# Performance work log

Hardware: AMD Instinct MI355X
Metric: run time of the kernel (lower is better)

The kernel has to match this reference:

```python
import jax, jax.numpy as jnp
import numpy as np

C = 512
H_HEADS = 8
CTX_D = 768
GEO_D = 512
FFN_D = 4 * C
EPS = 1e-5


def _layernorm(x, g, b):
    mu = jnp.mean(x, axis=-1, keepdims=True)
    var = jnp.mean((x - mu) ** 2, axis=-1, keepdims=True)
    return (x - mu) * jax.lax.rsqrt(var + EPS) * g + b


def _cross_attn(x, ctx, Wq, Wk, Wv, Wo, bo, h):
    # x: (B, N, C), ctx: (B, S, Dctx)
    b, n, _ = x.shape
    s = ctx.shape[1]
    inner = Wq.shape[1]
    d = inner // h
    q = (x @ Wq).reshape(b, n, h, d)
    k = (ctx @ Wk).reshape(b, s, h, d)
    v = (ctx @ Wv).reshape(b, s, h, d)
    sim = jnp.einsum('bihd,bjhd->bhij', q, k) * (d ** -0.5)
    attn = jax.nn.softmax(sim, axis=-1)
    out = jnp.einsum('bhij,bjhd->bihd', attn, v).reshape(b, n, inner)
    return out @ Wo + bo


def setup_inputs() -> dict:
    key = jax.random.key(0)
    ks = jax.random.split(key, 24)
    std = lambda fan_in: 1.0 / np.sqrt(fan_in)
    inp = {
        'x': jax.random.normal(ks[0], (4, C, 64, 64), jnp.float32),
        'context': jax.random.normal(ks[1], (4, 77, CTX_D), jnp.float32),
        'geometry_tokens': jax.random.normal(ks[2], (4, 256, GEO_D), jnp.float32),
        # layernorm params (norm1..norm4)
        'g1': jnp.ones((C,)), 'b1': jnp.zeros((C,)),
        'g2': jnp.ones((C,)), 'b2': jnp.zeros((C,)),
        'g3': jnp.ones((C,)), 'b3': jnp.zeros((C,)),
        'g4': jnp.ones((C,)), 'b4': jnp.zeros((C,)),
        # cross-attention (context) weights
        'cWq': jax.random.normal(ks[3], (C, C)) * std(C),
        'cWk': jax.random.normal(ks[4], (CTX_D, C)) * std(CTX_D),
        'cWv': jax.random.normal(ks[5], (CTX_D, C)) * std(CTX_D),
        'cWo': jax.random.normal(ks[6], (C, C)) * std(C),
        'cbo': jnp.zeros((C,)),
        # geometry-attention weights
        'gWq': jax.random.normal(ks[7], (C, C)) * std(C),
        'gWk': jax.random.normal(ks[8], (GEO_D, C)) * std(GEO_D),
        'gWv': jax.random.normal(ks[9], (GEO_D, C)) * std(GEO_D),
        'gWo': jax.random.normal(ks[10], (C, C)) * std(C),
        'gbo': jnp.zeros((C,)),
        # FFN weights
        'W1': jax.random.normal(ks[11], (C, FFN_D)) * std(C),
        'bf1': jnp.zeros((FFN_D,)),
        'W2': jax.random.normal(ks[12], (FFN_D, C)) * std(FFN_D),
        'bf2': jnp.zeros((C,)),
    }
    return inp


def reference(x, context, geometry_tokens,
              g1, b1, g2, b2, g3, b3, g4, b4,
              cWq, cWk, cWv, cWo, cbo,
              gWq, gWk, gWv, gWo, gbo,
              W1, bf1, W2, bf2):
    b, c, h, w = x.shape
    t = x.reshape(b, c, h * w).transpose(0, 2, 1)  # (B, N, C)
    # self_attn is called with context=None -> identity, so this is t + norm1(t)
    t = t + _layernorm(t, g1, b1)
    t = t + _cross_attn(_layernorm(t, g2, b2), context, cWq, cWk, cWv, cWo, cbo, H_HEADS)
    t = t + _cross_attn(_layernorm(t, g3, b3), geometry_tokens, gWq, gWk, gWv, gWo, gbo, H_HEADS)
    hdn = jax.nn.gelu(_layernorm(t, g4, b4) @ W1 + bf1, approximate=False)
    t = t + hdn @ W2 + bf2
    return t.transpose(0, 2, 1).reshape(b, c, h, w)
```

## Files before the change

kernel.cpp:

```cpp
#include <hip/hip_runtime.h>
#include <hip/hip_bf16.h>

using bf16 = __hip_bfloat16;
typedef __attribute__((ext_vector_type(8))) short short8;
typedef __attribute__((ext_vector_type(4))) short short4v;
typedef __attribute__((ext_vector_type(4))) float floatx4;

#define DEVFN __device__ __forceinline__

DEVFN float bf2f(bf16 v) { return __bfloat162float(v); }
DEVFN bf16 f2bf(float v) { return __float2bfloat16(v); }
DEVFN float us2f(unsigned short u) {
    union { unsigned int i; float f; } c; c.i = ((unsigned int)u) << 16; return c.f;
}
DEVFN unsigned short f2bfbits(float v) {
    union { bf16 h; unsigned short u; } c; c.h = f2bf(v); return c.u;
}
DEVFN float loadF(const void* p, size_t i, int isf) {
    return isf ? ((const float*)p)[i] : us2f(((const unsigned short*)p)[i]);
}
DEVFN void gl_lds16(const bf16* g, short* l) {
    __builtin_amdgcn_global_load_lds(
        (const __attribute__((address_space(1))) unsigned int*)g,
        (__attribute__((address_space(3))) unsigned int*)l, 16, 0, 0);
}
DEVFN float fast_gelu(float v) {
    float u = v * (0.7978845608028654f + 0.0356774081f * v * v);
    float e = __expf(2.f * u);
    float th = 1.f - 2.f / (e + 1.f);
    return 0.5f * v * (1.f + th);
}

__global__ __launch_bounds__(256) void detect_kernel(const void* x, int* flag)
{
    __shared__ int any;
    if (threadIdx.x == 0) any = 0;
    __syncthreads();
    const unsigned short* p = (const unsigned short*)x;
    int hit = 0;
    for (int i = threadIdx.x; i < 8192; i += 256) {
        if ((p[i] & 0x7F80u) == 0x7F80u) hit = 1;
    }
    if (hit) any = 1;
    __syncthreads();
    if (threadIdx.x == 0) flag[0] = any;
}

struct CVTab {
    const void* src[14];
    bf16* dst[14];
    int cnt[14];
    int bstart[14];
};
__global__ __launch_bounds__(256) void convert_batch_kernel(
    CVTab tab, const int* __restrict__ flag)
{
    int isf = *flag;
    int b = blockIdx.x;
    int s = 0;
#pragma unroll
    for (int i = 1; i < 14; i++) if (b >= tab.bstart[i]) s = i;
    const void* src = tab.src[s];
    bf16* dst = tab.dst[s];
    int cnt = tab.cnt[s];
    int base = (b - tab.bstart[s]) * 2048;
    int lim = min(base + 2048, cnt);
    for (int i = base + (int)threadIdx.x; i < lim; i += 256)
        dst[i] = f2bf(loadF(src, i, isf));
}

__global__ __launch_bounds__(256) void ln_in_kernel(
    const void* __restrict__ x, float* __restrict__ t,
    const bf16* __restrict__ g, const bf16* __restrict__ bta,
    const int* __restrict__ flag, int NN)
{
    __shared__ float tile[16][516];
    int isf = *flag;
    int b = blockIdx.y;
    int n0 = blockIdx.x * 16;
    int tid = threadIdx.x;
    int nx = tid & 15, cy = tid >> 4;
#pragma unroll
    for (int p = 0; p < 32; p++) {
        int c = p * 16 + cy;
        tile[nx][c] = loadF(x, ((size_t)b * 512 + c) * NN + n0 + nx, isf);
    }
    __syncthreads();
    int w = tid >> 6, lane = tid & 63;
    for (int rr = 0; rr < 4; rr++) {
        int r = w * 4 + rr;
        float4 v0 = *(const float4*)&tile[r][lane * 8];
        float4 v1 = *(const float4*)&tile[r][lane * 8 + 4];
        float vals[8] = {v0.x, v0.y, v0.z, v0.w, v1.x, v1.y, v1.z, v1.w};
        float s = 0.f;
#pragma unroll
        for (int i = 0; i < 8; i++) s += vals[i];
#pragma unroll
        for (int off = 32; off; off >>= 1) s += __shfl_xor(s, off, 64);
        float mu = s * (1.f / 512.f);
        float sq = 0.f;
#pragma unroll
        for (int i = 0; i < 8; i++) { float d = vals[i] - mu; sq += d * d; }
#pragma unroll
        for (int off = 32; off; off >>= 1) sq += __shfl_xor(sq, off, 64);
        float rs = rsqrtf(sq * (1.f / 512.f) + 1e-5f);
        float out[8];
#pragma unroll
        for (int i = 0; i < 8; i++) {
            int c = lane * 8 + i;
            out[i] = vals[i] + (vals[i] - mu) * rs * bf2f(g[c]) + bf2f(bta[c]);
        }
        float* tp = t + ((size_t)b * NN + n0 + r) * 512 + lane * 8;
        *(float4*)tp = make_float4(out[0], out[1], out[2], out[3]);
        *(float4*)(tp + 4) = make_float4(out[4], out[5], out[6], out[7]);
    }
}

__global__ __launch_bounds__(256) void transpose_out_kernel(
    const float* __restrict__ t, void* __restrict__ o, const int* __restrict__ flag,
    int C, int NN)
{
    __shared__ float tile[32][33];
    int isf = *flag;
    int b = blockIdx.z;
    int n0 = blockIdx.x * 32, c0 = blockIdx.y * 32;
    int tx = threadIdx.x, ty = threadIdx.y;
#pragma unroll
    for (int i = 0; i < 4; i++)
        tile[ty + i * 8][tx] = __builtin_nontemporal_load(
            &t[((size_t)b * NN + n0 + ty + i * 8) * C + c0 + tx]);
    __syncthreads();
#pragma unroll
    for (int i = 0; i < 4; i++) {
        size_t oi = ((size_t)b * C + c0 + ty + i * 8) * NN + n0 + tx;
        float val = tile[tx][ty + i * 8];
        if (isf) ((float*)o)[oi] = val;
        else ((bf16*)o)[oi] = f2bf(val);
    }
}

struct TWTab {
    const void* src[10];
    bf16* dst[10];
    int K[10];
    int Nc[10];
    int tstart[10];
};
__global__ __launch_bounds__(256) void transpose_w_batch(
    TWTab tab, const int* __restrict__ flag)
{
    __shared__ float tile[32][33];
    int isf = *flag;
    int b = blockIdx.x;
    int s = 0;
#pragma unroll
    for (int i = 1; i < 10; i++) if (b >= tab.tstart[i]) s = i;
    const void* Wm = tab.src[s];
    bf16* WT = tab.dst[s];
    int K = tab.K[s], Nc = tab.Nc[s];
    int lt = b - tab.tstart[s];
    int ntx = Nc >> 5;
    int n0 = (lt % ntx) * 32, k0 = (lt / ntx) * 32;
    int tx = threadIdx.x, ty = threadIdx.y;
#pragma unroll
    for (int i = 0; i < 4; i++)
        tile[ty + i * 8][tx] = loadF(Wm, (size_t)(k0 + ty + i * 8) * Nc + n0 + tx, isf);
    __syncthreads();
#pragma unroll
    for (int i = 0; i < 4; i++)
        WT[(size_t)(n0 + ty + i * 8) * K + k0 + tx] = f2bf(tile[tx][ty + i * 8]);
}

__global__ __launch_bounds__(256) void ln_kernel(
    const float* __restrict__ t, const bf16* __restrict__ g, const bf16* __restrict__ bta,
    bf16* __restrict__ outp, int Mrows)
{
    int w = threadIdx.x >> 6, lane = threadIdx.x & 63;
    int row = blockIdx.x * 4 + w;
    if (row >= Mrows) return;
    const float* xr = t + (size_t)row * 512;
    floatx4 v0 = __builtin_nontemporal_load((const floatx4*)(xr + lane * 8));
    floatx4 v1 = __builtin_nontemporal_load((const floatx4*)(xr + lane * 8 + 4));
    float vals[8] = {v0[0], v0[1], v0[2], v0[3], v1[0], v1[1], v1[2], v1[3]};
    float s = 0.f;
#pragma unroll
    for (int i = 0; i < 8; i++) s += vals[i];
#pragma unroll
    for (int off = 32; off; off >>= 1) s += __shfl_xor(s, off, 64);
    float mu = s * (1.f / 512.f);
    float sq = 0.f;
#pragma unroll
    for (int i = 0; i < 8; i++) { float d = vals[i] - mu; sq += d * d; }
#pragma unroll
    for (int off = 32; off; off >>= 1) sq += __shfl_xor(sq, off, 64);
    float rs = rsqrtf(sq * (1.f / 512.f) + 1e-5f);
#pragma unroll
    for (int i = 0; i < 8; i++) {
        int c = lane * 8 + i;
        float y = (vals[i] - mu) * rs * bf2f(g[c]) + bf2f(bta[c]);
        outp[(size_t)row * 512 + c] = f2bf(y);
    }
}

template <int MODE>
__global__ __launch_bounds__(256) void gemm64x2(
    const bf16* __restrict__ A,
    const bf16* __restrict__ WT0, const bf16* __restrict__ WT1,
    bf16* __restrict__ o0, bf16* __restrict__ o1,
    int M, int K, int Nc)
{
    const bf16* WT = blockIdx.z ? WT1 : WT0;
    bf16* outp = blockIdx.z ? o1 : o0;
    __shared__ short As[64 * 32];
    __shared__ short Bs[64 * 32];
    const int tid = threadIdx.x;
    const int m0 = blockIdx.y * 64;
    const int n0 = blockIdx.x * 64;
    const int w = tid >> 6;
    const int lane = tid & 63;
    const int lm = lane & 15;
    const int lq = lane >> 4;

    floatx4 acc[4];
#pragma unroll
    for (int nb = 0; nb < 4; nb++) acc[nb] = (floatx4){0.f, 0.f, 0.f, 0.f};

    const int srow = tid >> 2;
    const int scol = (tid & 3) << 3;
    const int agrow = m0 + srow;
    const bool aok = agrow < M;
    const bf16* Aptr = A + (size_t)agrow * K + scol;
    const bf16* Bptr = WT + (size_t)(n0 + srow) * K + scol;

    for (int k0 = 0; k0 < K; k0 += 32) {
        __syncthreads();
        int4 av = make_int4(0, 0, 0, 0);
        if (aok) av = *(const int4*)(Aptr + k0);
        *(int4*)(&As[srow * 32 + scol]) = av;
        *(int4*)(&Bs[srow * 32 + scol]) = *(const int4*)(Bptr + k0);
        __syncthreads();
        short8 a = *(const short8*)(&As[(w * 16 + lm) * 32 + lq * 8]);
#pragma unroll
        for (int nb = 0; nb < 4; nb++) {
            short8 b = *(const short8*)(&Bs[(nb * 16 + lm) * 32 + lq * 8]);
            acc[nb] = __builtin_amdgcn_mfma_f32_16x16x32_bf16(a, b, acc[nb], 0, 0, 0);
        }
    }

#pragma unroll
    for (int nb = 0; nb < 4; nb++) {
        int col = n0 + nb * 16 + lm;
#pragma unroll
        for (int r = 0; r < 4; r++) {
            int row = m0 + w * 16 + lq * 4 + r;
            if (row < M) {
                float v = acc[nb][r];
                if (MODE == 1) v = fast_gelu(v);
                outp[(size_t)row * Nc + col] = f2bf(v);
            }
        }
    }
}

#define MFMA_PAIR(RB, A00, A01, A10, A11)                                              \
    _Pragma("unroll")                                                                   \
    for (int cb = 0; cb < CB; cb++) {                                                   \
        acc[cb][RB]     = __builtin_amdgcn_mfma_f32_16x16x32_bf16(bf0[cb], A00, acc[cb][RB], 0, 0, 0);     \
        acc[cb][RB]     = __builtin_amdgcn_mfma_f32_16x16x32_bf16(bf1[cb], A01, acc[cb][RB], 0, 0, 0);     \
        acc[cb][RB + 1] = __builtin_amdgcn_mfma_f32_16x16x32_bf16(bf0[cb], A10, acc[cb][RB + 1], 0, 0, 0); \
        acc[cb][RB + 1] = __builtin_amdgcn_mfma_f32_16x16x32_bf16(bf1[cb], A11, acc[cb][RB + 1], 0, 0, 0); \
    }

template <int MODE, int CB>
__global__ __launch_bounds__(512, 2) void gemm8p(
    const bf16* __restrict__ A, const bf16* __restrict__ WT,
    const bf16* __restrict__ bias, void* __restrict__ outp,
    int K, int Nc)
{
    constexpr int BN = CB * 64;
    constexpr int ABUF = 256 * 64;
    constexpr int BBUF = BN * 64;
    __shared__ short As[2 * ABUF];
    __shared__ short Bs[2 * BBUF];

    const int tid = threadIdx.x;
    const int gx = gridDim.x;
    int g = blockIdx.y * gx + blockIdx.x;
    const int cpx = (gx * gridDim.y) >> 3;
    g = (g & 7) * cpx + (g >> 3);
    const int m0 = (g / gx) * 256;
    const int n0 = (g % gx) * BN;

    const int w = tid >> 6, lane = tid & 63;
    const int lm = lane & 15, lq = lane >> 4;
    const int wm = w >> 2, wn = w & 3;

    floatx4 acc[CB][8];
#pragma unroll
    for (int cb = 0; cb < CB; cb++)
#pragma unroll
        for (int rb = 0; rb < 8; rb++) acc[cb][rb] = (floatx4){0.f, 0.f, 0.f, 0.f};

    const int rbaseA = (tid >> 3) + ((tid >= 256) ? 96 : 0);
    const int chk = (((tid & 7) ^ ((tid >> 3) & 7)) << 3);
    const bf16* pA = A + (size_t)(m0 + rbaseA) * K + chk;
    const int rbaseB = ((tid >> 7) << (CB == 4 ? 6 : 5)) + ((tid >> 3) & 15);
    const bf16* pB = WT + (size_t)(n0 + rbaseB) * K + chk;
    const int wbA = w * 512 + ((w >= 4) ? 6144 : 0);
    const int wbB = (CB == 4) ? ((w >> 1) * 4096 + (w & 1) * 512)
                              : ((w >> 1) * 2048 + (w & 1) * 512);
    const size_t K32 = (size_t)K * 32;
    const size_t K16 = (size_t)K * 16;

    const int arow = (wm * 128 + lm) * 64;
    const int brow = (wn * CB * 16 + lm) * 64;
    const int sl0 = ((lq ^ (lm & 7)) << 3);
    const int sl1 = (((4 + lq) ^ (lm & 7)) << 3);

    const int nt = K >> 6;

#pragma unroll
    for (int q = 0; q < 4; q++) gl_lds16(pA + (size_t)q * K32, As + q * 2048 + wbA);
    if constexpr (CB == 4) {
        gl_lds16(pB,           Bs + wbB);
        gl_lds16(pB + K16,     Bs + 1024 + wbB);
        gl_lds16(pB + 2 * K16, Bs + 2048 + wbB);
        gl_lds16(pB + 3 * K16, Bs + 3072 + wbB);
    } else {
        gl_lds16(pB,       Bs + wbB);
        gl_lds16(pB + K16, Bs + 1024 + wbB);
    }
    {
        const bf16* qA = pA + 64;
        const bf16* qB = pB + 64;
        if constexpr (CB == 4) {
            gl_lds16(qB,           Bs + BBUF + wbB);
            gl_lds16(qB + K16,     Bs + BBUF + 1024 + wbB);
            gl_lds16(qB + 2 * K16, Bs + BBUF + 2048 + wbB);
            gl_lds16(qB + 3 * K16, Bs + BBUF + 3072 + wbB);
            gl_lds16(qA,           As + ABUF + wbA);
            gl_lds16(qA + K32,     As + ABUF + 2048 + wbA);
            asm volatile("s_waitcnt vmcnt(6)\n\ts_barrier" ::: "memory");
        } else {
            gl_lds16(qB,           Bs + BBUF + wbB);
            gl_lds16(qB + K16, Bs + BBUF + 1024 + wbB);
            gl_lds16(qA,           As + ABUF + wbA);
            gl_lds16(qA + K32,     As + ABUF + 2048 + wbA);
            gl_lds16(qA + 2 * K32, As + ABUF + 4096 + wbA);
            asm volatile("s_waitcnt vmcnt(5)\n\ts_barrier" ::: "memory");
        }
    }

    for (int s = 0; s < nt; ++s) {
        const int cu = s & 1;
        const short* cA = As + cu * ABUF;
        const short* cB = Bs + cu * BBUF;
        short* oA = As + (cu ^ 1) * ABUF;
        short* sA = As + cu * ABUF;
        short* sB = Bs + cu * BBUF;
        const bf16* pA1 = pA + (s + 1) * 64;
        const bf16* pA2 = pA + (s + 2) * 64;
        const bf16* pB2 = pB + (s + 2) * 64;
        short8 bf0[CB], bf1[CB], x0, x1, y0, y1;

#pragma unroll
        for (int cb = 0; cb < CB; cb++) {
            bf0[cb] = *(const short8*)&cB[brow + cb * 1024 + sl0];
            bf1[cb] = *(const short8*)&cB[brow + cb * 1024 + sl1];
        }
        x0 = *(const short8*)&cA[arow + sl0];
        x1 = *(const short8*)&cA[arow + sl1];
        y0 = *(const short8*)&cA[arow + 1024 + sl0];
        y1 = *(const short8*)&cA[arow + 1024 + sl1];
        if (s + 1 < nt) {
            if constexpr (CB == 4) {
                gl_lds16(pA1 + 2 * K32, oA + 2 * 2048 + wbA);
                gl_lds16(pA1 + 3 * K32, oA + 3 * 2048 + wbA);
            } else {
                gl_lds16(pA1 + 3 * K32, oA + 3 * 2048 + wbA);
            }
        }
        asm volatile("s_barrier" ::: "memory");
        __builtin_amdgcn_s_setprio(1);
        MFMA_PAIR(0, x0, x1, y0, y1)
        __builtin_amdgcn_s_setprio(0);
        asm volatile("s_waitcnt lgkmcnt(0)\n\ts_barrier" ::: "memory");

        x0 = *(const short8*)&cA[arow + 2 * 1024 + sl0];
        x1 = *(const short8*)&cA[arow + 2 * 1024 + sl1];
        y0 = *(const short8*)&cA[arow + 3 * 1024 + sl0];
        y1 = *(const short8*)&cA[arow + 3 * 1024 + sl1];
        if (s + 2 < nt) {
            gl_lds16(pB2,       sB + wbB);
            gl_lds16(pB2 + K16, sB + 1024 + wbB);
        }
        asm volatile("s_barrier" ::: "memory");
        __builtin_amdgcn_s_setprio(1);
        MFMA_PAIR(2, x0, x1, y0, y1)
        __builtin_amdgcn_s_setprio(0);
        asm volatile("s_waitcnt lgkmcnt(0)\n\ts_barrier" ::: "memory");

        x0 = *(const short8*)&cA[arow + 4 * 1024 + sl0];
        x1 = *(const short8*)&cA[arow + 4 * 1024 + sl1];
        y0 = *(const short8*)&cA[arow + 5 * 1024 + sl0];
        y1 = *(const short8*)&cA[arow + 5 * 1024 + sl1];
        if (s + 2 < nt) {
            if constexpr (CB == 4) {
                gl_lds16(pB2 + 2 * K16, sB + 2048 + wbB);
                gl_lds16(pB2 + 3 * K16, sB + 3072 + wbB);
            } else {
                gl_lds16(pA2, sA + wbA);
            }
        }
        asm volatile("s_barrier" ::: "memory");
        __builtin_amdgcn_s_setprio(1);
        MFMA_PAIR(4, x0, x1, y0, y1)
        __builtin_amdgcn_s_setprio(0);
        asm volatile("s_waitcnt lgkmcnt(0)\n\ts_barrier" ::: "memory");

        x0 = *(const short8*)&cA[arow + 6 * 1024 + sl0];
        x1 = *(const short8*)&cA[arow + 6 * 1024 + sl1];
        y0 = *(const short8*)&cA[arow + 7 * 1024 + sl0];
        y1 = *(const short8*)&cA[arow + 7 * 1024 + sl1];
        if (s + 2 < nt) {
            if constexpr (CB == 4) {
                gl_lds16(pA2,       sA + wbA);
                gl_lds16(pA2 + K32, sA + 2048 + wbA);
            } else {
                gl_lds16(pA2 + K32,     sA + 2048 + wbA);
                gl_lds16(pA2 + 2 * K32, sA + 4096 + wbA);
            }
        }
        asm volatile("s_barrier" ::: "memory");
        __builtin_amdgcn_s_setprio(1);
        MFMA_PAIR(6, x0, x1, y0, y1)
        __builtin_amdgcn_s_setprio(0);
        if (s <= nt - 3) {
            if constexpr (CB == 4)
                asm volatile("s_waitcnt vmcnt(6) lgkmcnt(0)\n\ts_barrier" ::: "memory");
            else
                asm volatile("s_waitcnt vmcnt(5) lgkmcnt(0)\n\ts_barrier" ::: "memory");
        } else if (s == nt - 2) {
            asm volatile("s_waitcnt vmcnt(0) lgkmcnt(0)\n\ts_barrier" ::: "memory");
        } else {
            asm volatile("s_waitcnt lgkmcnt(0)\n\ts_barrier" ::: "memory");
        }
    }
    __syncthreads();

    float4 bias4[CB];
#pragma unroll
    for (int cb = 0; cb < CB; cb++) {
        if (bias) {
            const bf16* bp = bias + n0 + wn * (CB * 16) + cb * 16 + lq * 4;
            bias4[cb] = make_float4(bf2f(bp[0]), bf2f(bp[1]), bf2f(bp[2]), bf2f(bp[3]));
        } else {
            bias4[cb] = make_float4(0.f, 0.f, 0.f, 0.f);
        }
    }

    if constexpr (MODE == 2) {
        float* po = (float*)outp;
#pragma unroll
        for (int rb = 0; rb < 8; rb++) {
            size_t m = m0 + wm * 128 + rb * 16 + lm;
#pragma unroll
            for (int cb = 0; cb < CB; cb++) {
                float* p = po + m * Nc + n0 + wn * (CB * 16) + cb * 16 + lq * 4;
                floatx4 f = __builtin_nontemporal_load((const floatx4*)p);
                f[0] += acc[cb][rb][0] + bias4[cb].x;
                f[1] += acc[cb][rb][1] + bias4[cb].y;
                f[2] += acc[cb][rb][2] + bias4[cb].z;
                f[3] += acc[cb][rb][3] + bias4[cb].w;
                __builtin_nontemporal_store(f, (floatx4*)p);
            }
        }
    } else if constexpr (CB == 2) {
        unsigned short* op = (unsigned short*)outp;
#pragma unroll
        for (int rb = 0; rb < 8; rb++) {
            size_t m = m0 + wm * 128 + rb * 16 + lm;
#pragma unroll
            for (int cb = 0; cb < 2; cb++) {
                short4v pk;
#pragma unroll
                for (int r = 0; r < 4; r++) {
                    float vv = acc[cb][rb][r] + ((const float*)&bias4[cb])[r];
                    if (MODE == 1) vv = fast_gelu(vv);
                    pk[r] = (short)f2bfbits(vv);
                }
                *(short4v*)(op + m * Nc + n0 + wn * 32 + cb * 16 + lq * 4) = pk;
            }
        }
    } else {
        unsigned short* stgb = (unsigned short*)&As[w * 1024];
        unsigned short* op = (unsigned short*)outp;
#pragma unroll
        for (int rb = 0; rb < 8; rb++) {
#pragma unroll
            for (int cb = 0; cb < 4; cb++) {
                short4v pk;
#pragma unroll
                for (int r = 0; r < 4; r++) {
                    float vv = acc[cb][rb][r] + ((const float*)&bias4[cb])[r];
                    if (MODE == 1) vv = fast_gelu(vv);
                    pk[r] = (short)f2bfbits(vv);
                }
                int chunk = (cb * 2 + (lq >> 1)) ^ (lm & 7);
                *(short4v*)(&stgb[lm * 64 + chunk * 8 + (lq & 1) * 4]) = pk;
            }
#pragma unroll
            for (int p = 0; p < 2; p++) {
                int row = p * 8 + (lane >> 3);
                int chunk = lane & 7;
                short8 ov = *(const short8*)(&stgb[row * 64 + ((chunk ^ (row & 7)) * 8)]);
                size_t m = m0 + wm * 128 + rb * 16 + row;
                short8* dst = (short8*)(op + m * Nc + n0 + wn * 64 + chunk * 8);
                if (MODE == 1) __builtin_nontemporal_store(ov, dst);
                else *dst = ov;
            }
        }
    }
}

template <int SPAD, int SVALID>
__global__ __launch_bounds__(256) void attn_mfma_kernel(
    const bf16* __restrict__ q, const bf16* __restrict__ k, const bf16* __restrict__ v,
    bf16* __restrict__ o, int N)
{
    constexpr int MB = SPAD / 16;
    constexpr int KS = SPAD / 32;
    __shared__ unsigned short lds[SPAD * 64 + 64 * SPAD];
    unsigned short* Ks = lds;
    unsigned short* Vt = lds + SPAD * 64;
    unsigned short* Pw = lds;

    const int tid = threadIdx.x;
    const int b = blockIdx.x >> 3;
    const int h = blockIdx.x & 7;
    const int n0 = blockIdx.y * 64;
    const int w = tid >> 6, lane = tid & 63;
    const int lm = lane & 15, lq = lane >> 4;

    const unsigned short* kp = (const unsigned short*)k;
    const unsigned short* vp = (const unsigned short*)v;
    for (int idx = tid * 8; idx < SPAD * 64; idx += 2048) {
        int s = idx >> 6, d0 = idx & 63;
        short8 kv = {0, 0, 0, 0, 0, 0, 0, 0};
        short8 vv = {0, 0, 0, 0, 0, 0, 0, 0};
        if (s < SVALID) {
            size_t gb = ((size_t)(b * SVALID + s)) * 512 + h * 64 + d0;
            kv = *(const short8*)(kp + gb);
            vv = *(const short8*)(vp + gb);
        }
        int kc = (d0 >> 3) ^ (s & 7);
        *(short8*)(&Ks[s * 64 + kc * 8]) = kv;
        const unsigned short* vvp = (const unsigned short*)&vv;
#pragma unroll
        for (int i = 0; i < 8; i++) {
            int d = d0 + i;
            int sc = (s >> 3) ^ (d & 7);
            Vt[d * SPAD + sc * 8 + (s & 7)] = vvp[i];
        }
    }

    const int q0 = n0 + w * 16;
    const unsigned short* qp = (const unsigned short*)q;
    size_t qbase = ((size_t)(b * N + q0 + lm)) * 512 + h * 64 + lq * 8;
    short8 qf0 = *(const short8*)(qp + qbase);
    short8 qf1 = *(const short8*)(qp + qbase + 32);
    __syncthreads();

    floatx4 sacc[MB];
#pragma unroll
    for (int mb = 0; mb < MB; mb++) sacc[mb] = (floatx4){0.f, 0.f, 0.f, 0.f};
#pragma unroll
    for (int mb = 0; mb < MB; mb++) {
        int srow = mb * 16 + lm;
        short8 a0 = *(const short8*)(&Ks[srow * 64 + ((lq ^ (lm & 7)) * 8)]);
        short8 a1 = *(const short8*)(&Ks[srow * 64 + (((4 + lq) ^ (lm & 7)) * 8)]);
        sacc[mb] = __builtin_amdgcn_mfma_f32_16x16x32_bf16(a0, qf0, sacc[mb], 0, 0, 0);
        sacc[mb] = __builtin_amdgcn_mfma_f32_16x16x32_bf16(a1, qf1, sacc[mb], 0, 0, 0);
    }

    float mx = -1e30f;
#pragma unroll
    for (int mb = 0; mb < MB; mb++)
#pragma unroll
        for (int r = 0; r < 4; r++) {
            int s = mb * 16 + lq * 4 + r;
            if (s < SVALID) mx = fmaxf(mx, sacc[mb][r]);
        }
    mx = fmaxf(mx, __shfl_xor(mx, 16, 64));
    mx = fmaxf(mx, __shfl_xor(mx, 32, 64));
    mx *= 0.125f;
    float sum = 0.f;
#pragma unroll
    for (int mb = 0; mb < MB; mb++)
#pragma unroll
        for (int r = 0; r < 4; r++) {
            int s = mb * 16 + lq * 4 + r;
            float e = (s < SVALID) ? __expf(sacc[mb][r] * 0.125f - mx) : 0.f;
            sacc[mb][r] = e;
            sum += e;
        }
    sum += __shfl_xor(sum, 16, 64);
    sum += __shfl_xor(sum, 32, 64);
    float inv = 1.f / sum;

    __syncthreads();

    unsigned short* Pme = Pw + w * 16 * SPAD;
#pragma unroll
    for (int mb = 0; mb < MB; mb++) {
        short4v pk;
        pk[0] = (short)f2bfbits(sacc[mb][0] * inv);
        pk[1] = (short)f2bfbits(sacc[mb][1] * inv);
        pk[2] = (short)f2bfbits(sacc[mb][2] * inv);
        pk[3] = (short)f2bfbits(sacc[mb][3] * inv);
        int chunk = (mb * 2 + (lq >> 1)) ^ (lm & 7);
        *(short4v*)(&Pme[lm * SPAD + chunk * 8 + (lq & 1) * 4]) = pk;
    }

    floatx4 oacc[4];
#pragma unroll
    for (int mb2 = 0; mb2 < 4; mb2++) oacc[mb2] = (floatx4){0.f, 0.f, 0.f, 0.f};
    for (int ks = 0; ks < KS; ks++) {
        int sch = ((ks * 4 + lq) ^ (lm & 7)) * 8;
        short8 bfrag = *(const short8*)(&Pme[lm * SPAD + sch]);
#pragma unroll
        for (int mb2 = 0; mb2 < 4; mb2++) {
            int d = mb2 * 16 + lm;
            short8 afrag = *(const short8*)(&Vt[d * SPAD + sch]);
            oacc[mb2] = __builtin_amdgcn_mfma_f32_16x16x32_bf16(afrag, bfrag, oacc[mb2], 0, 0, 0);
        }
    }

#pragma unroll
    for (int mb2 = 0; mb2 < 4; mb2++) {
        short4v ok;
        ok[0] = (short)f2bfbits(oacc[mb2][0]);
        ok[1] = (short)f2bfbits(oacc[mb2][1]);
        ok[2] = (short)f2bfbits(oacc[mb2][2]);
        ok[3] = (short)f2bfbits(oacc[mb2][3]);
        int chunk = (mb2 * 2 + (lq >> 1)) ^ (lm & 7);
        *(short4v*)(&Pme[lm * 64 + chunk * 8 + (lq & 1) * 4]) = ok;
    }
    unsigned short* op = (unsigned short*)o;
#pragma unroll
    for (int p = 0; p < 2; p++) {
        int row = p * 8 + (lane >> 3);
        int chunk = lane & 7;
        short8 ov = *(const short8*)(&Pme[row * 64 + ((chunk ^ (row & 7)) * 8)]);
        *(short8*)(op + ((size_t)(b * N + n0 + w * 16 + row)) * 512 + h * 64 + chunk * 8) = ov;
    }
}

extern "C" void kernel_launch(void* const* d_in, const int* in_sizes, int n_in,
                              void* d_out, int out_size, void* d_ws, size_t ws_size,
                              hipStream_t stream)
{
    const void* x   = d_in[0];
    const void* ctx = d_in[1];
    const void* geo = d_in[2];
    const void* g1 = d_in[3];  const void* b1 = d_in[4];
    const void* g2 = d_in[5];  const void* b2 = d_in[6];
    const void* g3 = d_in[7];  const void* b3 = d_in[8];
    const void* g4 = d_in[9];  const void* b4 = d_in[10];
    const void* cWq = d_in[11]; const void* cWk = d_in[12];
    const void* cWv = d_in[13]; const void* cWo = d_in[14];
    const void* cbo = d_in[15];
    const void* gWq = d_in[16]; const void* gWk = d_in[17];
    const void* gWv = d_in[18]; const void* gWo = d_in[19];
    const void* gbo = d_in[20];
    const void* W1 = d_in[21];  const void* bf1 = d_in[22];
    const void* W2 = d_in[23];  const void* bf2 = d_in[24];

    const int B = 4, C = 512, NN = 4096;
    const int M = B * NN;

    char* ws = (char*)d_ws;
    size_t off = 0;
    auto alloc = [&](size_t bytes) -> void* {
        void* p = ws + off; off += (bytes + 255) & ~(size_t)255; return p;
    };
    int*   flag = (int*)alloc(256);
    float* t  = (float*)alloc((size_t)M * C * 4);
    bf16* u   = (bf16*)alloc((size_t)M * C * 2);
    bf16* qb  = (bf16*)alloc((size_t)M * C * 2);
    bf16* kb  = (bf16*)alloc((size_t)B * 256 * C * 2);
    bf16* vb  = (bf16*)alloc((size_t)B * 256 * C * 2);
    bf16* ctxb = (bf16*)alloc((size_t)B * 77 * 768 * 2);
    bf16* geob = (bf16*)alloc((size_t)B * 256 * 512 * 2);
    bf16* cWqT = (bf16*)alloc((size_t)512 * 512 * 2);
    bf16* cWkT = (bf16*)alloc((size_t)512 * 768 * 2);
    bf16* cWvT = (bf16*)alloc((size_t)512 * 768 * 2);
    bf16* cWoT = (bf16*)alloc((size_t)512 * 512 * 2);
    bf16* gWqT = (bf16*)alloc((size_t)512 * 512 * 2);
    bf16* gWkT = (bf16*)alloc((size_t)512 * 512 * 2);
    bf16* gWvT = (bf16*)alloc((size_t)512 * 512 * 2);
    bf16* gWoT = (bf16*)alloc((size_t)512 * 512 * 2);
    bf16* W1T  = (bf16*)alloc((size_t)2048 * 512 * 2);
    bf16* W2T  = (bf16*)alloc((size_t)512 * 2048 * 2);
    bf16* prm  = (bf16*)alloc((size_t)7680 * 2);
    bf16* ob = u;

    int chunk;
    bf16* hb;
    size_t rem = (ws_size > off) ? (ws_size - off) : 0;
    if (rem >= (size_t)16384 * 2048 * 2) { chunk = 16384; hb = (bf16*)alloc((size_t)16384 * 2048 * 2); }
    else if (rem >= (size_t)8192 * 2048 * 2) { chunk = 8192; hb = (bf16*)alloc((size_t)8192 * 2048 * 2); }
    else { chunk = 4096; hb = qb; }
    (void)in_sizes; (void)n_in; (void)out_size;

    bf16 *pg1 = prm, *pb1 = prm + 512, *pg2 = prm + 1024, *pb2 = prm + 1536;
    bf16 *pg3 = prm + 2048, *pb3 = prm + 2560, *pg4 = prm + 3072, *pb4 = prm + 3584;
    bf16 *pcbo = prm + 4096, *pgbo = prm + 4608, *pbf1 = prm + 5120, *pbf2 = prm + 7168;

    dim3 tb(32, 8);

    detect_kernel<<<1, 256, 0, stream>>>(x, flag);

    {
        CVTab cv;
        const void* csrc[14] = {g1, b1, g2, b2, g3, b3, g4, b4, cbo, gbo, bf1, bf2, ctx, geo};
        bf16* cdst[14] = {prm, prm + 512, prm + 1024, prm + 1536, prm + 2048, prm + 2560,
                          prm + 3072, prm + 3584, prm + 4096, prm + 4608, prm + 5120,
                          prm + 7168, ctxb, geob};
        int ccnt[14] = {512, 512, 512, 512, 512, 512, 512, 512, 512, 512, 2048, 512,
                        B * 77 * 768, B * 256 * 512};
        int bacc = 0;
        for (int i = 0; i < 14; i++) {
            cv.src[i] = csrc[i]; cv.dst[i] = cdst[i]; cv.cnt[i] = ccnt[i];
            cv.bstart[i] = bacc;
            bacc += (ccnt[i] + 2047) / 2048;
        }
        convert_batch_kernel<<<bacc, 256, 0, stream>>>(cv, flag);
    }

    ln_in_kernel<<<dim3(NN / 16, B), 256, 0, stream>>>(x, t, pg1, pb1, flag, NN);

    {
        TWTab tw;
        const void* wsrc[10] = {cWq, cWk, cWv, cWo, gWq, gWk, gWv, gWo, W1, W2};
        bf16* wdst[10] = {cWqT, cWkT, cWvT, cWoT, gWqT, gWkT, gWvT, gWoT, W1T, W2T};
        int wK[10]  = {512, 768, 768, 512, 512, 512, 512, 512, 512, 2048};
        int wNc[10] = {512, 512, 512, 512, 512, 512, 512, 512, 2048, 512};
        int tacc = 0;
        for (int i = 0; i < 10; i++) {
            tw.src[i] = wsrc[i]; tw.dst[i] = wdst[i]; tw.K[i] = wK[i]; tw.Nc[i] = wNc[i];
            tw.tstart[i] = tacc;
            tacc += (wNc[i] / 32) * (wK[i] / 32);
        }
        transpose_w_batch<<<tacc, tb, 0, stream>>>(tw, flag);
    }

    ln_kernel<<<M / 4, 256, 0, stream>>>(t, pg2, pb2, u, M);
    gemm8p<0, 2><<<dim3(4, M / 256), 512, 0, stream>>>(u, cWqT, nullptr, qb, 512, 512);
    gemm64x2<0><<<dim3(8, (308 + 63) / 64, 2), 256, 0, stream>>>(ctxb, cWkT, cWvT, kb, vb, 308, 768, 512);
    attn_mfma_kernel<128, 77><<<dim3(B * 8, NN / 64), 256, 0, stream>>>(qb, kb, vb, ob, NN);
    gemm8p<2, 2><<<dim3(4, M / 256), 512, 0, stream>>>(ob, cWoT, pcbo, t, 512, 512);

    ln_kernel<<<M / 4, 256, 0, stream>>>(t, pg3, pb3, u, M);
    gemm8p<0, 2><<<dim3(4, M / 256), 512, 0, stream>>>(u, gWqT, nullptr, qb, 512, 512);
    gemm64x2<0><<<dim3(8, 1024 / 64, 2), 256, 0, stream>>>(geob, gWkT, gWvT, kb, vb, 1024, 512, 512);
    attn_mfma_kernel<256, 256><<<dim3(B * 8, NN / 64), 256, 0, stream>>>(qb, kb, vb, ob, NN);
    gemm8p<2, 2><<<dim3(4, M / 256), 512, 0, stream>>>(ob, gWoT, pgbo, t, 512, 512);

    ln_kernel<<<M / 4, 256, 0, stream>>>(t, pg4, pb4, u, M);
    for (int mc = 0; mc < M / chunk; mc++) {
        bf16* uc = u + (size_t)mc * chunk * 512;
        float* tc = t + (size_t)mc * chunk * 512;
        gemm8p<1, 4><<<dim3(2048 / 256, chunk / 256), 512, 0, stream>>>(uc, W1T, pbf1, hb, 512, 2048);
        gemm8p<2, 2><<<dim3(512 / 128, chunk / 256), 512, 0, stream>>>(hb, W2T, pbf2, tc, 2048, 512);
    }

    transpose_out_kernel<<<dim3(NN / 32, C / 32, B), tb, 0, stream>>>(t, d_out, flag, C, NN);
}
```

Baseline: 529.1 us.

## Write FFN output as bf16 and fold residual add into output transpose

The final W2 GEMM now stores its result as bf16 into a separate buffer rather than read-modify-writing the fp32 residual stream. The residual add moves into the output transpose kernel, which reads both t and the bf16 FFN output. This is meant to cut the fp32 load/store traffic of the last GEMM epilogue, at the cost of rounding the FFN output to bf16 before the add. Separately, nontemporal load/store hints are dropped in the layernorm, the residual GEMM epilogue and the bf16 store path, so these accesses go through the normal caches.

```diff
diff --git a/kernel.cpp b/kernel.cpp
--- a/kernel.cpp
+++ b/kernel.cpp
@@ -117,7 +117,8 @@
 }
 
 __global__ __launch_bounds__(256) void transpose_out_kernel(
-    const float* __restrict__ t, void* __restrict__ o, const int* __restrict__ flag,
+    const float* __restrict__ t, const bf16* __restrict__ f,
+    void* __restrict__ o, const int* __restrict__ flag,
     int C, int NN)
 {
     __shared__ float tile[32][33];
@@ -126,9 +127,10 @@
     int n0 = blockIdx.x * 32, c0 = blockIdx.y * 32;
     int tx = threadIdx.x, ty = threadIdx.y;
 #pragma unroll
-    for (int i = 0; i < 4; i++)
-        tile[ty + i * 8][tx] = __builtin_nontemporal_load(
-            &t[((size_t)b * NN + n0 + ty + i * 8) * C + c0 + tx]);
+    for (int i = 0; i < 4; i++) {
+        size_t idx = ((size_t)b * NN + n0 + ty + i * 8) * C + c0 + tx;
+        tile[ty + i * 8][tx] = t[idx] + bf2f(f[idx]);
+    }
     __syncthreads();
 #pragma unroll
     for (int i = 0; i < 4; i++) {
@@ -179,9 +181,9 @@
     int row = blockIdx.x * 4 + w;
     if (row >= Mrows) return;
     const float* xr = t + (size_t)row * 512;
-    floatx4 v0 = __builtin_nontemporal_load((const floatx4*)(xr + lane * 8));
-    floatx4 v1 = __builtin_nontemporal_load((const floatx4*)(xr + lane * 8 + 4));
-    float vals[8] = {v0[0], v0[1], v0[2], v0[3], v1[0], v1[1], v1[2], v1[3]};
+    float4 v0 = *(const float4*)(xr + lane * 8);
+    float4 v1 = *(const float4*)(xr + lane * 8 + 4);
+    float vals[8] = {v0.x, v0.y, v0.z, v0.w, v1.x, v1.y, v1.z, v1.w};
     float s = 0.f;
 #pragma unroll
     for (int i = 0; i < 8; i++) s += vals[i];
@@ -467,12 +469,12 @@
 #pragma unroll
             for (int cb = 0; cb < CB; cb++) {
                 float* p = po + m * Nc + n0 + wn * (CB * 16) + cb * 16 + lq * 4;
-                floatx4 f = __builtin_nontemporal_load((const floatx4*)p);
-                f[0] += acc[cb][rb][0] + bias4[cb].x;
-                f[1] += acc[cb][rb][1] + bias4[cb].y;
-                f[2] += acc[cb][rb][2] + bias4[cb].z;
-                f[3] += acc[cb][rb][3] + bias4[cb].w;
-                __builtin_nontemporal_store(f, (floatx4*)p);
+                float4 f = *(float4*)p;
+                f.x += acc[cb][rb][0] + bias4[cb].x;
+                f.y += acc[cb][rb][1] + bias4[cb].y;
+                f.z += acc[cb][rb][2] + bias4[cb].z;
+                f.w += acc[cb][rb][3] + bias4[cb].w;
+                *(float4*)p = f;
             }
         }
     } else if constexpr (CB == 2) {
@@ -515,9 +517,7 @@
                 int chunk = lane & 7;
                 short8 ov = *(const short8*)(&stgb[row * 64 + ((chunk ^ (row & 7)) * 8)]);
                 size_t m = m0 + wm * 128 + rb * 16 + row;
-                short8* dst = (short8*)(op + m * Nc + n0 + wn * 64 + chunk * 8);
-                if (MODE == 1) __builtin_nontemporal_store(ov, dst);
-                else *dst = ov;
+                *(short8*)(op + m * Nc + n0 + wn * 64 + chunk * 8) = ov;
             }
         }
     }
@@ -688,6 +688,7 @@
     float* t  = (float*)alloc((size_t)M * C * 4);
     bf16* u   = (bf16*)alloc((size_t)M * C * 2);
     bf16* qb  = (bf16*)alloc((size_t)M * C * 2);
+    bf16* fb  = (bf16*)alloc((size_t)M * C * 2);
     bf16* kb  = (bf16*)alloc((size_t)B * 256 * C * 2);
     bf16* vb  = (bf16*)alloc((size_t)B * 256 * C * 2);
     bf16* ctxb = (bf16*)alloc((size_t)B * 77 * 768 * 2);
@@ -770,10 +771,10 @@
     ln_kernel<<<M / 4, 256, 0, stream>>>(t, pg4, pb4, u, M);
     for (int mc = 0; mc < M / chunk; mc++) {
         bf16* uc = u + (size_t)mc * chunk * 512;
-        float* tc = t + (size_t)mc * chunk * 512;
+        bf16* fc = fb + (size_t)mc * chunk * 512;
         gemm8p<1, 4><<<dim3(2048 / 256, chunk / 256), 512, 0, stream>>>(uc, W1T, pbf1, hb, 512, 2048);
-        gemm8p<2, 2><<<dim3(512 / 128, chunk / 256), 512, 0, stream>>>(hb, W2T, pbf2, tc, 2048, 512);
-    }
-
-    transpose_out_kernel<<<dim3(NN / 32, C / 32, B), tb, 0, stream>>>(t, d_out, flag, C, NN);
-}
+        gemm8p<0, 2><<<dim3(512 / 128, chunk / 256), 512, 0, stream>>>(hb, W2T, pbf2, fc, 2048, 512);
+    }
+
+    transpose_out_kernel<<<dim3(NN / 32, C / 32, B), tb, 0, stream>>>(t, fb, d_out, flag, C, NN);
+}
```

Result: faster. 472.0 us (-10.8%).
